# Optimization experiments

Measured on AMD Instinct MI355X. Metric: run time of the kernel, lower is better.

## Reference

```python
import jax, jax.numpy as jnp
import numpy as np

HID = 1024
HEADS = 16
HEAD_DIM = HID // HEADS
LN_EPS = 1e-5  # nn.LayerNorm default (module's self.eps is unused by its LayerNorms)


def layer_norm(x, w, b):
    m = jnp.mean(x, axis=-1, keepdims=True)
    v = jnp.mean(jnp.square(x - m), axis=-1, keepdims=True)
    return (x - m) * jax.lax.rsqrt(v + LN_EPS) * w + b


def setup_inputs() -> dict:
    key = jax.random.key(0)
    ks = jax.random.split(key, 12)
    B, Nq, Nk = 2, 1024, 4096
    s = 1.0 / np.sqrt(HID)
    inp = {
        "queries": jax.random.normal(ks[0], (B, Nq, HID), jnp.float32),
        "kv_tokens": jax.random.normal(ks[1], (B, Nk, HID), jnp.float32),
        "query_type_ids": jax.random.randint(ks[2], (Nq,), 0, 3),
        "kv_type_ids": jax.random.randint(ks[3], (Nk,), 0, 3),
        "kv_padding_mask": jax.random.randint(ks[4], (B, Nk), 0, 2).astype(bool).at[:, 0].set(True),
        "Wq": jax.random.normal(ks[5], (HID, HID), jnp.float32) * s,
        "Wk": jax.random.normal(ks[6], (HID, HID), jnp.float32) * s,
        "Wv": jax.random.normal(ks[7], (HID, HID), jnp.float32) * s,
        "Wo": jax.random.normal(ks[8], (HID, HID), jnp.float32) * s,
        "qn_w": jnp.ones((HID,), jnp.float32), "qn_b": jnp.zeros((HID,), jnp.float32),
        "kvn_w": jnp.ones((HID,), jnp.float32), "kvn_b": jnp.zeros((HID,), jnp.float32),
        "on_w": jnp.ones((HID,), jnp.float32), "on_b": jnp.zeros((HID,), jnp.float32),
        "typed_bias": jax.random.normal(ks[9], (3, 3), jnp.float32) * 0.1,
    }
    return inp


def reference(queries, kv_tokens, query_type_ids, kv_type_ids, kv_padding_mask,
              Wq, Wk, Wv, Wo, qn_w, qn_b, kvn_w, kvn_b, on_w, on_b, typed_bias):
    B, Nq, D = queries.shape
    Nk = kv_tokens.shape[1]
    qn = layer_norm(queries, qn_w, qn_b)
    kvn = layer_norm(kv_tokens, kvn_w, kvn_b)
    # projections (torch Linear: x @ W.T), split heads -> [B, N, H, hd]
    q = (qn @ Wq.T).reshape(B, Nq, HEADS, HEAD_DIM)
    k = (kvn @ Wk.T).reshape(B, Nk, HEADS, HEAD_DIM)
    v = (kvn @ Wv.T).reshape(B, Nk, HEADS, HEAD_DIM)
    scale = 1.0 / jnp.sqrt(jnp.asarray(HEAD_DIM, queries.dtype))
    scores = jnp.einsum("bqhd,bkhd->bhqk", q, k) * scale  # [B,H,Nq,Nk]
    # additive mask: typed bias gather [Nq,Nk] + padding neg-inf [B,Nk]
    tbias = typed_bias[query_type_ids][:, kv_type_ids]  # [Nq,Nk]
    neg_inf = jnp.finfo(queries.dtype).min
    pad = jnp.where(kv_padding_mask[:, None, None, :], jnp.asarray(0.0, queries.dtype), neg_inf)
    attn = jax.nn.softmax(scores + tbias[None, None] + pad, axis=-1)
    out = jnp.einsum("bhqk,bkhd->bqhd", attn, v).reshape(B, Nq, D)
    out = out @ Wo.T
    return layer_norm(queries + out, on_w, on_b)
```

## Files before the change

### kernel.cpp

```cpp
#include <hip/hip_runtime.h>
#include <hip/hip_bf16.h>

#define HID   1024
#define NQ    1024
#define NK    4096
#define BB    2
#define HEADS 16
#define HD    64
#define LN_EPS 1e-5f
#define NEG_BIG (-1e9f)
#define SOFT_C 16.0f
#define KSPLIT 4
#define NKS   (NK / KSPLIT)

typedef __bf16 bf16_t;
typedef bf16_t bf16x8 __attribute__((ext_vector_type(8)));
typedef bf16_t bf16x4 __attribute__((ext_vector_type(4)));
typedef float  f32x4  __attribute__((ext_vector_type(4)));

__device__ inline f32x4 mfma16(bf16x8 a, bf16x8 b, f32x4 c) {
    return __builtin_amdgcn_mfma_f32_16x16x32_bf16(a, b, c, 0, 0, 0);
}

__device__ inline void async_copy16(const bf16_t* g, bf16_t* l) {
    __builtin_amdgcn_global_load_lds(
        (const __attribute__((address_space(1))) void*)g,
        (__attribute__((address_space(3))) void*)l, 16, 0, 0);
}

__device__ inline void load8f(const void* p, int idx, int fl, float* o) {
    if (fl) {
        bf16x8 v = *(const bf16x8*)((const bf16_t*)p + idx);
#pragma unroll
        for (int i = 0; i < 8; i++) o[i] = (float)v[i];
    } else {
        float4 a = *(const float4*)((const float*)p + idx);
        float4 b = *(const float4*)((const float*)p + idx + 4);
        o[0] = a.x; o[1] = a.y; o[2] = a.z; o[3] = a.w;
        o[4] = b.x; o[5] = b.y; o[6] = b.z; o[7] = b.w;
    }
}
__device__ inline void load4f(const void* p, int idx, int fl, float* o) {
    if (fl) {
        bf16x4 v = *(const bf16x4*)((const bf16_t*)p + idx);
#pragma unroll
        for (int i = 0; i < 4; i++) o[i] = (float)v[i];
    } else {
        float4 a = *(const float4*)((const float*)p + idx);
        o[0] = a.x; o[1] = a.y; o[2] = a.z; o[3] = a.w;
    }
}

__global__ void detect_kernel(const void* __restrict__ qnw,
                              const void* __restrict__ pad,
                              int* __restrict__ flags) {
    __shared__ int bad;
    if (threadIdx.x == 0) bad = 0;
    __syncthreads();
    const unsigned int* pw = (const unsigned int*)pad;
    int any = 0;
    for (int i = threadIdx.x; i < 2048; i += 256)
        if (pw[i] > 1u) any = 1;
    if (any) atomicOr(&bad, 1);
    __syncthreads();
    if (threadIdx.x == 0) {
        flags[0] = (*(const unsigned int*)qnw == 0x3F803F80u) ? 1 : 0;
        flags[1] = bad;
    }
}

__device__ inline float2 block_sum2(float a, float b) {
#pragma unroll
    for (int off = 32; off > 0; off >>= 1) {
        a += __shfl_down(a, off, 64);
        b += __shfl_down(b, off, 64);
    }
    __shared__ float sm[8];
    int w = threadIdx.x >> 6;
    if ((threadIdx.x & 63) == 0) { sm[w] = a; sm[w + 4] = b; }
    __syncthreads();
    float sa = sm[0] + sm[1] + sm[2] + sm[3];
    float sb = sm[4] + sm[5] + sm[6] + sm[7];
    return make_float2(sa, sb);
}

__global__ __launch_bounds__(256) void norm_rows_kernel(const void* __restrict__ x,
                                                        const void* __restrict__ lnw,
                                                        const void* __restrict__ lnb,
                                                        bf16_t* __restrict__ out,
                                                        const int* __restrict__ flags) {
    int fl = flags[0];
    int row = blockIdx.x;
    int t = threadIdx.x;
    float xf[4];
    load4f(x, row * HID + t * 4, fl, xf);
    float s = 0.f, s2 = 0.f;
#pragma unroll
    for (int i = 0; i < 4; i++) { s += xf[i]; s2 += xf[i] * xf[i]; }
    float2 sums = block_sum2(s, s2);
    float mean = sums.x * (1.0f / HID);
    float var  = fmaxf(sums.y * (1.0f / HID) - mean * mean, 0.f);
    float inv  = rsqrtf(var + LN_EPS);
    float wv[4], bv[4];
    load4f(lnw, t * 4, fl, wv);
    load4f(lnb, t * 4, fl, bv);
    bf16x4 o;
#pragma unroll
    for (int i = 0; i < 4; i++)
        o[i] = (bf16_t)((xf[i] - mean) * inv * wv[i] + bv[i]);
    *(bf16x4*)(out + (size_t)row * HID + t * 4) = o;
}

__global__ __launch_bounds__(256) void wconv_kernel(const void* __restrict__ w0,
                                                    const void* __restrict__ w1,
                                                    const void* __restrict__ w2,
                                                    const void* __restrict__ w3,
                                                    bf16_t* __restrict__ out,
                                                    const int* __restrict__ flags) {
    int z = blockIdx.y;
    const void* in = (z == 0) ? w0 : (z == 1) ? w1 : (z == 2) ? w2 : w3;
    bf16_t* o = out + (size_t)z * HID * HID;
    int i = (blockIdx.x * 256 + threadIdx.x) * 8;
    if (flags[0]) {
        *(uint4*)(o + i) = *(const uint4*)((const bf16_t*)in + i);
    } else {
        float4 a = *(const float4*)((const float*)in + i);
        float4 b = *(const float4*)((const float*)in + i + 4);
        bf16x8 v;
        v[0] = (bf16_t)a.x; v[1] = (bf16_t)a.y; v[2] = (bf16_t)a.z; v[3] = (bf16_t)a.w;
        v[4] = (bf16_t)b.x; v[5] = (bf16_t)b.y; v[6] = (bf16_t)b.z; v[7] = (bf16_t)b.w;
        *(bf16x8*)(o + i) = v;
    }
}

__global__ __launch_bounds__(256) void final_ln_kernel(const void* __restrict__ q,
                                                       const float* __restrict__ o2a,
                                                       const float* __restrict__ o2b,
                                                       const void* __restrict__ w,
                                                       const void* __restrict__ bias,
                                                       void* __restrict__ y,
                                                       const int* __restrict__ flags) {
    int fl = flags[0];
    int row = blockIdx.x;
    int t = threadIdx.x;
    float qf[4];
    load4f(q, row * HID + t * 4, fl, qf);
    float4 oa = *(const float4*)(o2a + (size_t)row * HID + t * 4);
    float4 ob = *(const float4*)(o2b + (size_t)row * HID + t * 4);
    float xf[4] = { qf[0] + oa.x + ob.x, qf[1] + oa.y + ob.y,
                    qf[2] + oa.z + ob.z, qf[3] + oa.w + ob.w };
    float s = 0.f, s2 = 0.f;
#pragma unroll
    for (int i = 0; i < 4; i++) { s += xf[i]; s2 += xf[i] * xf[i]; }
    float2 sums = block_sum2(s, s2);
    float mean = sums.x * (1.0f / HID);
    float var  = fmaxf(sums.y * (1.0f / HID) - mean * mean, 0.f);
    float inv  = rsqrtf(var + LN_EPS);
    float wv[4], bv[4];
    load4f(w, t * 4, fl, wv);
    load4f(bias, t * 4, fl, bv);
    if (fl) {
        bf16x4 out;
#pragma unroll
        for (int i = 0; i < 4; i++)
            out[i] = (bf16_t)((xf[i] - mean) * inv * wv[i] + bv[i]);
        *(bf16x4*)((bf16_t*)y + (size_t)row * HID + t * 4) = out;
    } else {
        float4 out;
        out.x = (xf[0] - mean) * inv * wv[0] + bv[0];
        out.y = (xf[1] - mean) * inv * wv[1] + bv[1];
        out.z = (xf[2] - mean) * inv * wv[2] + bv[2];
        out.w = (xf[3] - mean) * inv * wv[3] + bv[3];
        *(float4*)((float*)y + (size_t)row * HID + t * 4) = out;
    }
}

__global__ __launch_bounds__(256) void maskc_kernel(const int* __restrict__ kt,
                                                    const void* __restrict__ pad,
                                                    const void* __restrict__ tb,
                                                    float* __restrict__ mc,
                                                    const int* __restrict__ flags) {
    int fl = flags[0], padbyte = flags[1];
    int i = blockIdx.x * 256 + threadIdx.x;
    int tq  = i / (BB * NK);
    int rem = i - tq * (BB * NK);
    int b   = rem >> 12;
    int key = rem & (NK - 1);
    int ti = tq * 3 + kt[key];
    float v = fl ? (float)((const bf16_t*)tb)[ti] : ((const float*)tb)[ti];
    v -= SOFT_C;
    bool ok = padbyte ? (((const unsigned char*)pad)[b * NK + key] != 0)
                      : (((const int*)pad)[b * NK + key] != 0);
    if (!ok) v = NEG_BIG;
    mc[i] = v;
}

__global__ __launch_bounds__(256) void gemm_qkv(const bf16_t* __restrict__ Aq,
                                                const bf16_t* __restrict__ Akv,
                                                const bf16_t* __restrict__ Wq,
                                                const bf16_t* __restrict__ Wkv,
                                                bf16_t* __restrict__ qp,
                                                bf16_t* __restrict__ kp,
                                                bf16_t* __restrict__ vT) {
    const int K = HID;
    __shared__ bf16_t As[128 * 32];
    __shared__ bf16_t Bs[128 * 32];
    int bid = blockIdx.x;
    bool isQ = bid < 128;
    const bf16_t* A; const bf16_t* W; int row0, col0;
    if (isQ) { A = Aq;  W = Wq;  row0 = (bid >> 3) * 128;  col0 = (bid & 7) * 128; }
    else     { int b2 = bid - 128;
               A = Akv; W = Wkv; row0 = (b2 >> 4) * 128;   col0 = (b2 & 15) * 128; }
    int t = threadIdx.x;
    int wave = t >> 6, lane = t & 63, quad = lane >> 4, l15 = lane & 15;
    int wr = wave >> 1, wc = wave & 1;

    int j0 = wave * 2;
    int srow = (lane >> 2);
    int skc  = (lane & 3) * 8;
    const bf16_t* Ag0 = A + (size_t)(row0 + 16 * j0 + srow) * K + skc;
    const bf16_t* Ag1 = Ag0 + (size_t)16 * K;
    const bf16_t* Bg0 = W + (size_t)(col0 + 16 * j0 + srow) * K + skc;
    const bf16_t* Bg1 = Bg0 + (size_t)16 * K;
    bf16_t* Asl0 = &As[j0 * 512];
    bf16_t* Asl1 = &As[j0 * 512 + 512];
    bf16_t* Bsl0 = &Bs[j0 * 512];
    bf16_t* Bsl1 = &Bs[j0 * 512 + 512];

    int aoff = (wr * 64 + l15) * 32 + quad * 8;
    int boff = (wc * 64 + l15) * 32 + quad * 8;

    f32x4 zero = {0.f, 0.f, 0.f, 0.f};
    f32x4 acc[4][4];
#pragma unroll
    for (int mt = 0; mt < 4; mt++)
#pragma unroll
        for (int nt = 0; nt < 4; nt++) acc[mt][nt] = zero;

    for (int k0 = 0; k0 < K; k0 += 32) {
        async_copy16(Ag0 + k0, Asl0);
        async_copy16(Ag1 + k0, Asl1);
        async_copy16(Bg0 + k0, Bsl0);
        async_copy16(Bg1 + k0, Bsl1);
        __syncthreads();
        bf16x8 a[4], b[4];
#pragma unroll
        for (int mt = 0; mt < 4; mt++) a[mt] = *(const bf16x8*)(&As[aoff + mt * 512]);
// ... 51 lines not shown
    int j0 = wave * 2;
    int srow = (lane >> 2);
    int skc  = (lane & 3) * 8;
    const bf16_t* Ag0 = A + (size_t)(row0 + 16 * j0 + srow) * K + skc;
    const bf16_t* Ag1 = Ag0 + (size_t)16 * K;
    const bf16_t* Bg0 = W + (size_t)(col0 + 16 * j0 + srow) * K + skc;
    const bf16_t* Bg1 = Bg0 + (size_t)16 * K;
    bf16_t* Asl0 = &As[j0 * 512];
    bf16_t* Asl1 = &As[j0 * 512 + 512];
    bf16_t* Bsl0 = &Bs[j0 * 512];
    bf16_t* Bsl1 = &Bs[j0 * 512 + 512];

    int aoff = (wr * 64 + l15) * 32 + quad * 8;
    int boff = (wc * 64 + l15) * 32 + quad * 8;

    f32x4 zero = {0.f, 0.f, 0.f, 0.f};
    f32x4 acc[4][4];
#pragma unroll
    for (int mt = 0; mt < 4; mt++)
#pragma unroll
        for (int nt = 0; nt < 4; nt++) acc[mt][nt] = zero;

    for (int k0 = kbeg; k0 < kend; k0 += 32) {
        async_copy16(Ag0 + k0, Asl0);
        async_copy16(Ag1 + k0, Asl1);
        async_copy16(Bg0 + k0, Bsl0);
        async_copy16(Bg1 + k0, Bsl1);
        __syncthreads();
        bf16x8 a[4], b[4];
#pragma unroll
        for (int mt = 0; mt < 4; mt++) a[mt] = *(const bf16x8*)(&As[aoff + mt * 512]);
#pragma unroll
        for (int nt = 0; nt < 4; nt++) b[nt] = *(const bf16x8*)(&Bs[boff + nt * 512]);
#pragma unroll
        for (int mt = 0; mt < 4; mt++)
#pragma unroll
            for (int nt = 0; nt < 4; nt++)
                acc[mt][nt] = mfma16(a[mt], b[nt], acc[mt][nt]);
        __syncthreads();
    }

#pragma unroll
    for (int mt = 0; mt < 4; mt++)
#pragma unroll
        for (int nt = 0; nt < 4; nt++) {
            int gr = row0 + wr * 64 + mt * 16 + quad * 4;
            int gc = col0 + wc * 64 + nt * 16 + l15;
#pragma unroll
            for (int r = 0; r < 4; r++)
                Co[(size_t)(gr + r) * HID + gc] = acc[mt][nt][r];
        }
}

__global__ __launch_bounds__(256) void attn_kernel(const bf16_t* __restrict__ q,
                                                   const bf16_t* __restrict__ kmat,
                                                   const bf16_t* __restrict__ vT,
                                                   const int* __restrict__ qt,
                                                   const float* __restrict__ mc,
                                                   bf16_t* __restrict__ Opart,
                                                   float* __restrict__ lpart) {
    int q0 = blockIdx.x * 64;
    int h  = blockIdx.y;
    int zz = blockIdx.z;
    int b  = zz >> 2;
    int split = zz & (KSPLIT - 1);
    int t = threadIdx.x, wave = t >> 6, lane = t & 63, quad = lane >> 4, l15 = lane & 15;

    __shared__ bf16_t Ks[2][64 * 64];
    __shared__ bf16_t Vs[2][64 * 64];

    const bf16_t* qbase = q + ((size_t)(b * NQ + q0 + wave * 16 + l15)) * HID + h * HD + quad * 8;
    bf16x8 aq0 = *(const bf16x8*)(qbase);
    bf16x8 aq1 = *(const bf16x8*)(qbase + 32);

    int qi = q0 + wave * 16 + l15;
    const float* mrow = mc + ((size_t)qt[qi] * BB + b) * NK;

    f32x4 zero = {0.f, 0.f, 0.f, 0.f};
    f32x4 O[4] = {zero, zero, zero, zero};
    float l_ = 0.f;

    int kt_beg = split * NKS;

    int srow = wave * 16 + (lane >> 2);
    int sc2  = (lane & 3) * 2;
    int vsw = srow & 7;
    int vl0 = srow * 64 + ((sc2)     ^ vsw) * 8;
    int vl1 = srow * 64 + ((sc2 + 1) ^ vsw) * 8;
    int prow = (srow & 0x23) | ((srow & 4) << 2) | ((srow >> 1) & 0x0C);
    int ksw = prow & 7;
    int kl0 = prow * 64 + ((sc2)     ^ ksw) * 8;
    int kl1 = prow * 64 + ((sc2 + 1) ^ ksw) * 8;

    const bf16_t* kgp = kmat + ((size_t)(b * NK + kt_beg + srow)) * HID + h * HD + sc2 * 8;
    const bf16_t* vgp = vT + ((size_t)(b * HID + h * HD + srow)) * NK + kt_beg + sc2 * 8;

    int fx = l15 & 7;
    int fA = l15 * 64 + ((quad) ^ fx) * 8;
    int fB = l15 * 64 + ((quad | 4) ^ fx) * 8;

    {
        uint4 ka = *(const uint4*)(kgp), kb = *(const uint4*)(kgp + 8);
        uint4 va = *(const uint4*)(vgp), vb = *(const uint4*)(vgp + 8);
        *(uint4*)&Ks[0][kl0] = ka; *(uint4*)&Ks[0][kl1] = kb;
        *(uint4*)&Vs[0][vl0] = va; *(uint4*)&Vs[0][vl1] = vb;
        kgp += 64 * HID; vgp += 64;
    }

    for (int it = 0; it < NKS / 64; ++it) {
        int cur = it & 1;
        __syncthreads();
        bool more = (it + 1 < NKS / 64);
        uint4 ka, kb, va, vb;
        if (more) {
            ka = *(const uint4*)(kgp); kb = *(const uint4*)(kgp + 8);
            va = *(const uint4*)(vgp); vb = *(const uint4*)(vgp + 8);
            kgp += 64 * HID; vgp += 64;
        }
        int kt0 = kt_beg + it * 64;
        float4 mk4[4];
#pragma unroll
        for (int nt = 0; nt < 4; nt++)
            mk4[nt] = *(const float4*)(mrow + kt0 + ((nt >> 1) << 5) + (quad << 3) + ((nt & 1) << 2));
        const bf16_t* Kc = Ks[cur];
        const bf16_t* Vc = Vs[cur];
        f32x4 s4[4] = {zero, zero, zero, zero};
#pragma unroll
        for (int nt = 0; nt < 4; nt++) {
            bf16x8 k0 = *(const bf16x8*)(Kc + nt * 1024 + fA);
            bf16x8 k1 = *(const bf16x8*)(Kc + nt * 1024 + fB);
            s4[nt] = mfma16(k0, aq0, s4[nt]);
            s4[nt] = mfma16(k1, aq1, s4[nt]);
        }
        bf16x8 pa0, pa1;
#pragma unroll
        for (int nt = 0; nt < 4; nt++) {
            const float* mkp = (const float*)&mk4[nt];
#pragma unroll
            for (int r = 0; r < 4; r++) {
                float p = __expf(fmaf(s4[nt][r], 0.125f, mkp[r]));
                l_ += p;
                bf16_t pb = (bf16_t)p;
                if (nt == 0)      pa0[r]     = pb;
                else if (nt == 1) pa0[r + 4] = pb;
                else if (nt == 2) pa1[r]     = pb;
                else              pa1[r + 4] = pb;
            }
        }
#pragma unroll
        for (int dt = 0; dt < 4; dt++) {
            bf16x8 v0 = *(const bf16x8*)(Vc + dt * 1024 + fA);
            bf16x8 v1 = *(const bf16x8*)(Vc + dt * 1024 + fB);
            O[dt] = mfma16(v0, pa0, O[dt]);
            O[dt] = mfma16(v1, pa1, O[dt]);
        }
        if (more) {
            int nxt = cur ^ 1;
            *(uint4*)&Ks[nxt][kl0] = ka; *(uint4*)&Ks[nxt][kl1] = kb;
            *(uint4*)&Vs[nxt][vl0] = va; *(uint4*)&Vs[nxt][vl1] = vb;
        }
    }

    size_t srow_base = (size_t)((split * BB + b) * HEADS + h) * NQ;
    float lf = l_;
    lf += __shfl_xor(lf, 16, 64);
    lf += __shfl_xor(lf, 32, 64);
    if (quad == 0) lpart[srow_base + qi] = lf;

    bf16_t* ob = &Ks[0][0] + wave * 1024;
#pragma unroll
    for (int dt = 0; dt < 4; dt++) {
        bf16x4 ov;
#pragma unroll
        for (int r = 0; r < 4; r++) ov[r] = (bf16_t)O[dt][r];
        *(bf16x4*)(ob + l15 * 64 + (((dt * 2 + (quad >> 1)) ^ fx) << 3) + ((quad & 1) << 2)) = ov;
    }
    int qq = lane >> 2, cc = lane & 3, sx = qq & 7;
    bf16x8 r0 = *(const bf16x8*)(ob + qq * 64 + (((cc * 2)     ^ sx) << 3));
    bf16x8 r1 = *(const bf16x8*)(ob + qq * 64 + (((cc * 2 + 1) ^ sx) << 3));
    size_t orow = (srow_base + (size_t)(q0 + wave * 16 + qq)) * HD + cc * 16;
    *(uint4*)(Opart + orow)     = *(uint4*)&r0;
    *(uint4*)(Opart + orow + 8) = *(uint4*)&r1;
}

__global__ __launch_bounds__(256) void combine_kernel(const bf16_t* __restrict__ Opart,
                                                      const float* __restrict__ lpart,
                                                      bf16_t* __restrict__ ctx) {
    int wave = threadIdx.x >> 6, lane = threadIdx.x & 63;
    int rid = blockIdx.x * 4 + wave;
    int b   = rid >> 14;
    int rem = rid & 16383;
    int h   = rem >> 10;
    int qi  = rem & 1023;
    float o = 0.f, l = 0.f;
#pragma unroll
    for (int s = 0; s < KSPLIT; s++) {
        size_t idx = (size_t)((s * BB + b) * HEADS + h) * NQ + qi;
        l += lpart[idx];
        o += (float)Opart[idx * HD + lane];
    }
    ctx[(size_t)(b * NQ + qi) * HID + h * HD + lane] = (bf16_t)(o / l);
}

extern "C" void kernel_launch(void* const* d_in, const int* in_sizes, int n_in,
                              void* d_out, int out_size, void* d_ws, size_t ws_size,
                              hipStream_t stream) {
    (void)in_sizes; (void)n_in; (void)out_size; (void)ws_size;
    const void* queries = d_in[0];
    const void* kv      = d_in[1];
    const int* qt       = (const int*)d_in[2];
    const int* kt       = (const int*)d_in[3];
    const void* pad     = d_in[4];
    const void* Wq   = d_in[5];
    const void* Wk   = d_in[6];
    const void* Wv   = d_in[7];
    const void* Wo   = d_in[8];
    const void* qn_w = d_in[9];
    const void* qn_b = d_in[10];
    const void* kvn_w = d_in[11];
    const void* kvn_b = d_in[12];
    const void* on_w = d_in[13];
    const void* on_b = d_in[14];
    const void* tb   = d_in[15];

    char* ws = (char*)d_ws;
    bf16_t* q_c  = (bf16_t*)(ws);
    bf16_t* kv_c = (bf16_t*)(ws + ((size_t)4  << 20));
    bf16_t* ctx  = (bf16_t*)(ws + ((size_t)4  << 20));
    bf16_t* Wq_c = (bf16_t*)(ws + ((size_t)20 << 20));
    bf16_t* Wk_c = (bf16_t*)(ws + ((size_t)22 << 20));
    bf16_t* Wv_c = (bf16_t*)(ws + ((size_t)24 << 20));
    bf16_t* Wo_c = (bf16_t*)(ws + ((size_t)26 << 20));
    bf16_t* qp   = (bf16_t*)(ws + ((size_t)28 << 20));
    bf16_t* kp   = (bf16_t*)(ws + ((size_t)32 << 20));
    float*  o2a  = (float*)(ws + ((size_t)32 << 20));
    float*  o2b  = (float*)(ws + ((size_t)40 << 20));
    bf16_t* vT   = (bf16_t*)(ws + ((size_t)48 << 20));
    float*  mc   = (float*)(ws + ((size_t)64 << 20));
    int*    flags = (int*)(ws + ((size_t)64 << 20) + (256 << 10));
    bf16_t* Opart = (bf16_t*)(ws + ((size_t)65 << 20));
    float*  lbuf  = (float*)(ws + ((size_t)82 << 20));

    detect_kernel<<<1, 256, 0, stream>>>(qn_w, pad, flags);
    norm_rows_kernel<<<BB * NQ, 256, 0, stream>>>(queries, qn_w, qn_b, q_c, flags);
    norm_rows_kernel<<<BB * NK, 256, 0, stream>>>(kv, kvn_w, kvn_b, kv_c, flags);
    wconv_kernel<<<dim3(512, 4), 256, 0, stream>>>(Wq, Wk, Wv, Wo, Wq_c, flags);
    maskc_kernel<<<(3 * BB * NK) / 256, 256, 0, stream>>>(kt, pad, tb, mc, flags);
    gemm_qkv<<<1152, 256, 0, stream>>>(q_c, kv_c, Wq_c, Wk_c, qp, kp, vT);
    attn_kernel<<<dim3(NQ / 64, HEADS, BB * KSPLIT), 256, 0, stream>>>(qp, kp, vT, qt, mc, Opart, lbuf);
    combine_kernel<<<(BB * HEADS * NQ) / 4, 256, 0, stream>>>(Opart, lbuf, ctx);
    gemm_o<<<dim3(16, 8, 2), 256, 0, stream>>>(ctx, Wo_c, o2a, o2b);
    final_ln_kernel<<<BB * NQ, 256, 0, stream>>>(queries, o2a, o2b, on_w, on_b, d_out, flags);
}
```

Baseline: 278.0 us.

## Deepen attention K/V prefetch pipeline, remap blocks for XCD locality, use exp2

The attention kernel's K/V tile loop now keeps two tiles of loads in flight in registers, unrolled by two with ping-pong LDS buffers. Mask loads are prefetched one tile ahead, and a lighter LDS-wait-plus-barrier replaces __syncthreads. The grid is flattened to 1D and remapped so consecutive blocks on the same XCD share a (head, batch, split) group for L2 reuse of K/V. The softmax switches to exp2 with log2e folded into the scale and the mask constants, which adds register pressure in exchange for hiding global-load latency.

```diff
diff --git a/kernel.cpp b/kernel.cpp
--- a/kernel.cpp
+++ b/kernel.cpp
@@ -12,6 +12,8 @@
 #define SOFT_C 16.0f
 #define KSPLIT 4
 #define NKS   (NK / KSPLIT)
+#define LOG2E 1.4426950408889634f
+#define QSCALE_L2E 0.18033688f
 
 typedef __bf16 bf16_t;
 typedef bf16_t bf16x8 __attribute__((ext_vector_type(8)));
@@ -28,18 +30,6 @@
         (__attribute__((address_space(3))) void*)l, 16, 0, 0);
 }
 
-__device__ inline void load8f(const void* p, int idx, int fl, float* o) {
-    if (fl) {
-        bf16x8 v = *(const bf16x8*)((const bf16_t*)p + idx);
-#pragma unroll
-        for (int i = 0; i < 8; i++) o[i] = (float)v[i];
-    } else {
-        float4 a = *(const float4*)((const float*)p + idx);
-        float4 b = *(const float4*)((const float*)p + idx + 4);
-        o[0] = a.x; o[1] = a.y; o[2] = a.z; o[3] = a.w;
-        o[4] = b.x; o[5] = b.y; o[6] = b.z; o[7] = b.w;
-    }
-}
 __device__ inline void load4f(const void* p, int idx, int fl, float* o) {
     if (fl) {
         bf16x4 v = *(const bf16x4*)((const bf16_t*)p + idx);
@@ -188,7 +178,7 @@
     int key = rem & (NK - 1);
     int ti = tq * 3 + kt[key];
     float v = fl ? (float)((const bf16_t*)tb)[ti] : ((const float*)tb)[ti];
-    v -= SOFT_C;
+    v = (v - SOFT_C) * LOG2E;
     bool ok = padbyte ? (((const unsigned char*)pad)[b * NK + key] != 0)
                       : (((const int*)pad)[b * NK + key] != 0);
     if (!ok) v = NEG_BIG;
@@ -357,10 +347,12 @@
                                                    const float* __restrict__ mc,
                                                    bf16_t* __restrict__ Opart,
                                                    float* __restrict__ lpart) {
-    int q0 = blockIdx.x * 64;
-    int h  = blockIdx.y;
-    int zz = blockIdx.z;
-    int b  = zz >> 2;
+    int d   = blockIdx.x;
+    int idx = ((d & 7) << 8) | (d >> 3);
+    int q0  = (idx & 15) * 64;
+    int h   = (idx >> 4) & 15;
+    int zz  = idx >> 8;
+    int b   = zz >> 2;
     int split = zz & (KSPLIT - 1);
     int t = threadIdx.x, wave = t >> 6, lane = t & 63, quad = lane >> 4, l15 = lane & 15;
 
@@ -379,6 +371,7 @@
     float l_ = 0.f;
 
     int kt_beg = split * NKS;
+    const int NT = NKS / 64;
 
     int srow = wave * 16 + (lane >> 2);
     int sc2  = (lane & 3) * 2;
@@ -390,73 +383,95 @@
     int kl0 = prow * 64 + ((sc2)     ^ ksw) * 8;
     int kl1 = prow * 64 + ((sc2 + 1) ^ ksw) * 8;
 
-    const bf16_t* kgp = kmat + ((size_t)(b * NK + kt_beg + srow)) * HID + h * HD + sc2 * 8;
-    const bf16_t* vgp = vT + ((size_t)(b * HID + h * HD + srow)) * NK + kt_beg + sc2 * 8;
+    const bf16_t* kbase = kmat + ((size_t)(b * NK + kt_beg + srow)) * HID + h * HD + sc2 * 8;
+    const bf16_t* vbase = vT + ((size_t)(b * HID + h * HD + srow)) * NK + kt_beg + sc2 * 8;
+    const float*  mbase = mrow + kt_beg + (quad << 3);
 
     int fx = l15 & 7;
     int fA = l15 * 64 + ((quad) ^ fx) * 8;
     int fB = l15 * 64 + ((quad | 4) ^ fx) * 8;
 
-    {
-        uint4 ka = *(const uint4*)(kgp), kb = *(const uint4*)(kgp + 8);
-        uint4 va = *(const uint4*)(vgp), vb = *(const uint4*)(vgp + 8);
-        *(uint4*)&Ks[0][kl0] = ka; *(uint4*)&Ks[0][kl1] = kb;
-        *(uint4*)&Vs[0][vl0] = va; *(uint4*)&Vs[0][vl1] = vb;
-        kgp += 64 * HID; vgp += 64;
-    }
-
-    for (int it = 0; it < NKS / 64; ++it) {
-        int cur = it & 1;
-        __syncthreads();
-        bool more = (it + 1 < NKS / 64);
-        uint4 ka, kb, va, vb;
-        if (more) {
-            ka = *(const uint4*)(kgp); kb = *(const uint4*)(kgp + 8);
-            va = *(const uint4*)(vgp); vb = *(const uint4*)(vgp + 8);
-            kgp += 64 * HID; vgp += 64;
-        }
-        int kt0 = kt_beg + it * 64;
-        float4 mk4[4];
-#pragma unroll
-        for (int nt = 0; nt < 4; nt++)
-            mk4[nt] = *(const float4*)(mrow + kt0 + ((nt >> 1) << 5) + (quad << 3) + ((nt & 1) << 2));
-        const bf16_t* Kc = Ks[cur];
-        const bf16_t* Vc = Vs[cur];
-        f32x4 s4[4] = {zero, zero, zero, zero};
-#pragma unroll
-        for (int nt = 0; nt < 4; nt++) {
-            bf16x8 k0 = *(const bf16x8*)(Kc + nt * 1024 + fA);
-            bf16x8 k1 = *(const bf16x8*)(Kc + nt * 1024 + fB);
-            s4[nt] = mfma16(k0, aq0, s4[nt]);
-            s4[nt] = mfma16(k1, aq1, s4[nt]);
-        }
-        bf16x8 pa0, pa1;
-#pragma unroll
-        for (int nt = 0; nt < 4; nt++) {
-            const float* mkp = (const float*)&mk4[nt];
-#pragma unroll
-            for (int r = 0; r < 4; r++) {
-                float p = __expf(fmaf(s4[nt][r], 0.125f, mkp[r]));
-                l_ += p;
-                bf16_t pb = (bf16_t)p;
-                if (nt == 0)      pa0[r]     = pb;
-                else if (nt == 1) pa0[r + 4] = pb;
-                else if (nt == 2) pa1[r]     = pb;
-                else              pa1[r + 4] = pb;
-            }
-        }
-#pragma unroll
-        for (int dt = 0; dt < 4; dt++) {
-            bf16x8 v0 = *(const bf16x8*)(Vc + dt * 1024 + fA);
-            bf16x8 v1 = *(const bf16x8*)(Vc + dt * 1024 + fB);
-            O[dt] = mfma16(v0, pa0, O[dt]);
-            O[dt] = mfma16(v1, pa1, O[dt]);
-        }
-        if (more) {
-            int nxt = cur ^ 1;
-            *(uint4*)&Ks[nxt][kl0] = ka; *(uint4*)&Ks[nxt][kl1] = kb;
-            *(uint4*)&Vs[nxt][vl0] = va; *(uint4*)&Vs[nxt][vl1] = vb;
-        }
+    uint4 kA0, kA1, vA0, vA1;
+    uint4 kB0, kB1, vB0, vB1;
+    float4 mA[4], mB[4];
+
+#define PKV(K0, K1, V0, V1, IT)                                              \
+    if ((IT) < NT) {                                                         \
+        const bf16_t* kp_ = kbase + (size_t)(IT) * 64 * HID;                 \
+        const bf16_t* vp_ = vbase + (size_t)(IT) * 64;                       \
+        K0 = *(const uint4*)(kp_); K1 = *(const uint4*)(kp_ + 8);            \
+        V0 = *(const uint4*)(vp_); V1 = *(const uint4*)(vp_ + 8);            \
+    }
+#define PM(M, IT)                                                            \
+    if ((IT) < NT) {                                                         \
+        const float* mp_ = mbase + (size_t)(IT) * 64;                        \
+        M[0] = *(const float4*)(mp_);                                        \
+        M[1] = *(const float4*)(mp_ + 4);                                    \
+        M[2] = *(const float4*)(mp_ + 32);                                   \
+        M[3] = *(const float4*)(mp_ + 36);                                   \
+    }
+#define WKV(BUF, K0, K1, V0, V1, IT)                                         \
+    if ((IT) < NT) {                                                         \
+        *(uint4*)&Ks[BUF][kl0] = K0; *(uint4*)&Ks[BUF][kl1] = K1;            \
+        *(uint4*)&Vs[BUF][vl0] = V0; *(uint4*)&Vs[BUF][vl1] = V1;            \
+    }
+#define BAR()                                                                \
+    {                                                                        \
+        asm volatile("s_waitcnt lgkmcnt(0)" ::: "memory");                   \
+        __builtin_amdgcn_s_barrier();                                        \
+    }
+#define COMPUTE(BUF, M)                                                      \
+    {                                                                        \
+        const bf16_t* Kc = Ks[BUF];                                          \
+        const bf16_t* Vc = Vs[BUF];                                          \
+        f32x4 s4[4] = {zero, zero, zero, zero};                              \
+        _Pragma("unroll")                                                    \
+        for (int nt = 0; nt < 4; nt++) {                                     \
+            bf16x8 k0 = *(const bf16x8*)(Kc + nt * 1024 + fA);               \
+            bf16x8 k1 = *(const bf16x8*)(Kc + nt * 1024 + fB);               \
+            s4[nt] = mfma16(k0, aq0, s4[nt]);                                \
+            s4[nt] = mfma16(k1, aq1, s4[nt]);                                \
+        }                                                                    \
+        bf16x8 pa0, pa1;                                                     \
+        _Pragma("unroll")                                                    \
+        for (int nt = 0; nt < 4; nt++) {                                     \
+            const float* mkp = (const float*)&M[nt];                         \
+            _Pragma("unroll")                                                \
+            for (int r = 0; r < 4; r++) {                                    \
+                float p = exp2f(fmaf(s4[nt][r], QSCALE_L2E, mkp[r]));        \
+                l_ += p;                                                     \
+                bf16_t pb = (bf16_t)p;                                       \
+                if (nt == 0)      pa0[r]     = pb;                           \
+                else if (nt == 1) pa0[r + 4] = pb;                           \
+                else if (nt == 2) pa1[r]     = pb;                           \
+                else              pa1[r + 4] = pb;                           \
+            }                                                                \
+        }                                                                    \
+        _Pragma("unroll")                                                    \
+        for (int dt = 0; dt < 4; dt++) {                                     \
+            bf16x8 v0 = *(const bf16x8*)(Vc + dt * 1024 + fA);               \
+            bf16x8 v1 = *(const bf16x8*)(Vc + dt * 1024 + fB);               \
+            O[dt] = mfma16(v0, pa0, O[dt]);                                  \
+            O[dt] = mfma16(v1, pa1, O[dt]);                                  \
+        }                                                                    \
+    }
+
+    PKV(kA0, kA1, vA0, vA1, 0);
+    WKV(0, kA0, kA1, vA0, vA1, 0);
+    PKV(kB0, kB1, vB0, vB1, 1);
+    PM(mA, 0);
+
+    for (int it = 0; it < NT; it += 2) {
+        PM(mB, it + 1);
+        PKV(kA0, kA1, vA0, vA1, it + 2);
+        BAR();
+        COMPUTE(0, mA);
+        WKV(1, kB0, kB1, vB0, vB1, it + 1);
+        PM(mA, it + 2);
+        PKV(kB0, kB1, vB0, vB1, it + 3);
+        BAR();
+        COMPUTE(1, mB);
+        WKV(0, kA0, kA1, vA0, vA1, it + 2);
     }
 
     size_t srow_base = (size_t)((split * BB + b) * HEADS + h) * NQ;
@@ -479,6 +494,11 @@
     size_t orow = (srow_base + (size_t)(q0 + wave * 16 + qq)) * HD + cc * 16;
     *(uint4*)(Opart + orow)     = *(uint4*)&r0;
     *(uint4*)(Opart + orow + 8) = *(uint4*)&r1;
+#undef PKV
+#undef PM
+#undef WKV
+#undef BAR
+#undef COMPUTE
 }
 
 __global__ __launch_bounds__(256) void combine_kernel(const bf16_t* __restrict__ Opart,
@@ -545,7 +565,7 @@
     wconv_kernel<<<dim3(512, 4), 256, 0, stream>>>(Wq, Wk, Wv, Wo, Wq_c, flags);
     maskc_kernel<<<(3 * BB * NK) / 256, 256, 0, stream>>>(kt, pad, tb, mc, flags);
     gemm_qkv<<<1152, 256, 0, stream>>>(q_c, kv_c, Wq_c, Wk_c, qp, kp, vT);
-    attn_kernel<<<dim3(NQ / 64, HEADS, BB * KSPLIT), 256, 0, stream>>>(qp, kp, vT, qt, mc, Opart, lbuf);
+    attn_kernel<<<dim3((NQ / 64) * HEADS * BB * KSPLIT), 256, 0, stream>>>(qp, kp, vT, qt, mc, Opart, lbuf);
     combine_kernel<<<(BB * HEADS * NQ) / 4, 256, 0, stream>>>(Opart, lbuf, ctx);
     gemm_o<<<dim3(16, 8, 2), 256, 0, stream>>>(ctx, Wo_c, o2a, o2b);
     final_ln_kernel<<<BB * NQ, 256, 0, stream>>>(queries, o2a, o2b, on_w, on_b, d_out, flags);
```

After: 292.7 us. +5.3%, slower.

## Single-buffer attention LDS, remap blocks across XCDs, use exp2 and wave priority

Applied to the files above, without the earlier changes.

Attention now keeps K/V in a single LDS buffer: register-prefetched tiles are written to LDS between two raw barriers, which halves LDS use so that 8 blocks per CU can be requested in launch bounds. The grid is flattened and remapped so that consecutive blocks sharing the same head and split land on the same XCD, aiming for better L2 reuse of K/V. Softmax switches to exp2, with log2(e) folded into the mask constants and the score scale, and s_setprio raises wave priority around the MFMA sections. The cost is an extra barrier per iteration and less overlap between LDS writes and compute. The unused load8f helper is removed.

```diff
diff --git a/kernel.cpp b/kernel.cpp
--- a/kernel.cpp
+++ b/kernel.cpp
@@ -12,6 +12,8 @@
 #define SOFT_C 16.0f
 #define KSPLIT 4
 #define NKS   (NK / KSPLIT)
+#define LOG2E 1.4426950408889634f
+#define QSCALE_L2E 0.18033688f
 
 typedef __bf16 bf16_t;
 typedef bf16_t bf16x8 __attribute__((ext_vector_type(8)));
@@ -28,18 +30,6 @@
         (__attribute__((address_space(3))) void*)l, 16, 0, 0);
 }
 
-__device__ inline void load8f(const void* p, int idx, int fl, float* o) {
-    if (fl) {
-        bf16x8 v = *(const bf16x8*)((const bf16_t*)p + idx);
-#pragma unroll
-        for (int i = 0; i < 8; i++) o[i] = (float)v[i];
-    } else {
-        float4 a = *(const float4*)((const float*)p + idx);
-        float4 b = *(const float4*)((const float*)p + idx + 4);
-        o[0] = a.x; o[1] = a.y; o[2] = a.z; o[3] = a.w;
-        o[4] = b.x; o[5] = b.y; o[6] = b.z; o[7] = b.w;
-    }
-}
 __device__ inline void load4f(const void* p, int idx, int fl, float* o) {
     if (fl) {
         bf16x4 v = *(const bf16x4*)((const bf16_t*)p + idx);
@@ -188,7 +178,7 @@
     int key = rem & (NK - 1);
     int ti = tq * 3 + kt[key];
     float v = fl ? (float)((const bf16_t*)tb)[ti] : ((const float*)tb)[ti];
-    v -= SOFT_C;
+    v = (v - SOFT_C) * LOG2E;
     bool ok = padbyte ? (((const unsigned char*)pad)[b * NK + key] != 0)
                       : (((const int*)pad)[b * NK + key] != 0);
     if (!ok) v = NEG_BIG;
@@ -350,22 +340,24 @@
         }
 }
 
-__global__ __launch_bounds__(256) void attn_kernel(const bf16_t* __restrict__ q,
-                                                   const bf16_t* __restrict__ kmat,
-                                                   const bf16_t* __restrict__ vT,
-                                                   const int* __restrict__ qt,
-                                                   const float* __restrict__ mc,
-                                                   bf16_t* __restrict__ Opart,
-                                                   float* __restrict__ lpart) {
-    int q0 = blockIdx.x * 64;
-    int h  = blockIdx.y;
-    int zz = blockIdx.z;
-    int b  = zz >> 2;
+__global__ __launch_bounds__(256, 8) void attn_kernel(const bf16_t* __restrict__ q,
+                                                      const bf16_t* __restrict__ kmat,
+                                                      const bf16_t* __restrict__ vT,
+                                                      const int* __restrict__ qt,
+                                                      const float* __restrict__ mc,
+                                                      bf16_t* __restrict__ Opart,
+                                                      float* __restrict__ lpart) {
+    int d   = blockIdx.x;
+    int idx = ((d & 7) << 8) | (d >> 3);
+    int q0  = (idx & 15) * 64;
+    int h   = (idx >> 4) & 15;
+    int zz  = idx >> 8;
+    int b   = zz >> 2;
     int split = zz & (KSPLIT - 1);
     int t = threadIdx.x, wave = t >> 6, lane = t & 63, quad = lane >> 4, l15 = lane & 15;
 
-    __shared__ bf16_t Ks[2][64 * 64];
-    __shared__ bf16_t Vs[2][64 * 64];
+    __shared__ bf16_t Ks[64 * 64];
+    __shared__ bf16_t Vs[64 * 64];
 
     const bf16_t* qbase = q + ((size_t)(b * NQ + q0 + wave * 16 + l15)) * HID + h * HD + quad * 8;
     bf16x8 aq0 = *(const bf16x8*)(qbase);
@@ -379,64 +371,64 @@
     float l_ = 0.f;
 
     int kt_beg = split * NKS;
+    const int NT = NKS / 64;
 
     int srow = wave * 16 + (lane >> 2);
     int sc2  = (lane & 3) * 2;
     int vsw = srow & 7;
-    int vl0 = srow * 64 + ((sc2)     ^ vsw) * 8;
-    int vl1 = srow * 64 + ((sc2 + 1) ^ vsw) * 8;
+    int vl0 = srow * 64 + ((sc2) ^ vsw) * 8;
+    int vl1 = vl0 ^ 8;
     int prow = (srow & 0x23) | ((srow & 4) << 2) | ((srow >> 1) & 0x0C);
     int ksw = prow & 7;
-    int kl0 = prow * 64 + ((sc2)     ^ ksw) * 8;
-    int kl1 = prow * 64 + ((sc2 + 1) ^ ksw) * 8;
+    int kl0 = prow * 64 + ((sc2) ^ ksw) * 8;
+    int kl1 = kl0 ^ 8;
 
     const bf16_t* kgp = kmat + ((size_t)(b * NK + kt_beg + srow)) * HID + h * HD + sc2 * 8;
     const bf16_t* vgp = vT + ((size_t)(b * HID + h * HD + srow)) * NK + kt_beg + sc2 * 8;
+    const float*  mbase = mrow + kt_beg + (quad << 3);
 
     int fx = l15 & 7;
     int fA = l15 * 64 + ((quad) ^ fx) * 8;
-    int fB = l15 * 64 + ((quad | 4) ^ fx) * 8;
-
-    {
-        uint4 ka = *(const uint4*)(kgp), kb = *(const uint4*)(kgp + 8);
-        uint4 va = *(const uint4*)(vgp), vb = *(const uint4*)(vgp + 8);
-        *(uint4*)&Ks[0][kl0] = ka; *(uint4*)&Ks[0][kl1] = kb;
-        *(uint4*)&Vs[0][vl0] = va; *(uint4*)&Vs[0][vl1] = vb;
-        kgp += 64 * HID; vgp += 64;
-    }
-
-    for (int it = 0; it < NKS / 64; ++it) {
-        int cur = it & 1;
-        __syncthreads();
-        bool more = (it + 1 < NKS / 64);
-        uint4 ka, kb, va, vb;
-        if (more) {
+    int fB = fA ^ 32;
+
+    uint4 ka = *(const uint4*)(kgp), kb = *(const uint4*)(kgp + 8);
+    uint4 va = *(const uint4*)(vgp), vb = *(const uint4*)(vgp + 8);
+    kgp += 64 * HID; vgp += 64;
+
+    for (int it = 0; it < NT; ++it) {
+        __builtin_amdgcn_s_barrier();
+        *(uint4*)&Ks[kl0] = ka; *(uint4*)&Ks[kl1] = kb;
+        *(uint4*)&Vs[vl0] = va; *(uint4*)&Vs[vl1] = vb;
+        asm volatile("s_waitcnt lgkmcnt(0)" ::: "memory");
+        __builtin_amdgcn_s_barrier();
+        if (it + 1 < NT) {
             ka = *(const uint4*)(kgp); kb = *(const uint4*)(kgp + 8);
             va = *(const uint4*)(vgp); vb = *(const uint4*)(vgp + 8);
             kgp += 64 * HID; vgp += 64;
         }
-        int kt0 = kt_beg + it * 64;
+        const float* mp = mbase + it * 64;
         float4 mk4[4];
-#pragma unroll
-        for (int nt = 0; nt < 4; nt++)
-            mk4[nt] = *(const float4*)(mrow + kt0 + ((nt >> 1) << 5) + (quad << 3) + ((nt & 1) << 2));
-        const bf16_t* Kc = Ks[cur];
-        const bf16_t* Vc = Vs[cur];
+        mk4[0] = *(const float4*)(mp);
+        mk4[1] = *(const float4*)(mp + 4);
+        mk4[2] = *(const float4*)(mp + 32);
+        mk4[3] = *(const float4*)(mp + 36);
         f32x4 s4[4] = {zero, zero, zero, zero};
+        __builtin_amdgcn_s_setprio(1);
 #pragma unroll
         for (int nt = 0; nt < 4; nt++) {
-            bf16x8 k0 = *(const bf16x8*)(Kc + nt * 1024 + fA);
-            bf16x8 k1 = *(const bf16x8*)(Kc + nt * 1024 + fB);
+            bf16x8 k0 = *(const bf16x8*)(Ks + nt * 1024 + fA);
+            bf16x8 k1 = *(const bf16x8*)(Ks + nt * 1024 + fB);
             s4[nt] = mfma16(k0, aq0, s4[nt]);
             s4[nt] = mfma16(k1, aq1, s4[nt]);
         }
+        __builtin_amdgcn_s_setprio(0);
         bf16x8 pa0, pa1;
 #pragma unroll
         for (int nt = 0; nt < 4; nt++) {
             const float* mkp = (const float*)&mk4[nt];
 #pragma unroll
             for (int r = 0; r < 4; r++) {
-                float p = __expf(fmaf(s4[nt][r], 0.125f, mkp[r]));
+                float p = exp2f(fmaf(s4[nt][r], QSCALE_L2E, mkp[r]));
                 l_ += p;
                 bf16_t pb = (bf16_t)p;
                 if (nt == 0)      pa0[r]     = pb;
@@ -445,18 +437,15 @@
                 else              pa1[r + 4] = pb;
             }
         }
+        __builtin_amdgcn_s_setprio(1);
 #pragma unroll
         for (int dt = 0; dt < 4; dt++) {
-            bf16x8 v0 = *(const bf16x8*)(Vc + dt * 1024 + fA);
-            bf16x8 v1 = *(const bf16x8*)(Vc + dt * 1024 + fB);
+            bf16x8 v0 = *(const bf16x8*)(Vs + dt * 1024 + fA);
+            bf16x8 v1 = *(const bf16x8*)(Vs + dt * 1024 + fB);
             O[dt] = mfma16(v0, pa0, O[dt]);
             O[dt] = mfma16(v1, pa1, O[dt]);
         }
-        if (more) {
-            int nxt = cur ^ 1;
-            *(uint4*)&Ks[nxt][kl0] = ka; *(uint4*)&Ks[nxt][kl1] = kb;
-            *(uint4*)&Vs[nxt][vl0] = va; *(uint4*)&Vs[nxt][vl1] = vb;
-        }
+        __builtin_amdgcn_s_setprio(0);
     }
 
     size_t srow_base = (size_t)((split * BB + b) * HEADS + h) * NQ;
@@ -465,7 +454,8 @@
     lf += __shfl_xor(lf, 32, 64);
     if (quad == 0) lpart[srow_base + qi] = lf;
 
-    bf16_t* ob = &Ks[0][0] + wave * 1024;
+    __syncthreads();
+    bf16_t* ob = &Ks[0] + wave * 1024;
 #pragma unroll
     for (int dt = 0; dt < 4; dt++) {
         bf16x4 ov;
@@ -545,7 +535,7 @@
     wconv_kernel<<<dim3(512, 4), 256, 0, stream>>>(Wq, Wk, Wv, Wo, Wq_c, flags);
     maskc_kernel<<<(3 * BB * NK) / 256, 256, 0, stream>>>(kt, pad, tb, mc, flags);
     gemm_qkv<<<1152, 256, 0, stream>>>(q_c, kv_c, Wq_c, Wk_c, qp, kp, vT);
-    attn_kernel<<<dim3(NQ / 64, HEADS, BB * KSPLIT), 256, 0, stream>>>(qp, kp, vT, qt, mc, Opart, lbuf);
+    attn_kernel<<<dim3((NQ / 64) * HEADS * BB * KSPLIT), 256, 0, stream>>>(qp, kp, vT, qt, mc, Opart, lbuf);
     combine_kernel<<<(BB * HEADS * NQ) / 4, 256, 0, stream>>>(Opart, lbuf, ctx);
     gemm_o<<<dim3(16, 8, 2), 256, 0, stream>>>(ctx, Wo_c, o2a, o2b);
     final_ln_kernel<<<BB * NQ, 256, 0, stream>>>(queries, o2a, o2b, on_w, on_b, d_out, flags);
```

New measurement: 537.1 us. 1.93x slower.

## Fuse prep kernels into one launch, use exp2 softmax, split attention by batch

Applied to the files above, without the earlier changes.

Merges the detect, both layernorm passes, the weight conversion and the mask-construction kernels into a single prep kernel. Dtype detection now happens inline in each kernel instead of through a flags buffer, which removes several launches and the serial dependency on the detect kernel. The mask is prescaled by log2(e) so the softmax can use exp2f with a folded scale constant. Attention is now launched as two half-size grids, one per batch, which adds a launch and may lower occupancy per grid.

```diff
diff --git a/kernel.cpp b/kernel.cpp
--- a/kernel.cpp
+++ b/kernel.cpp
@@ -12,6 +12,8 @@
 #define SOFT_C 16.0f
 #define KSPLIT 4
 #define NKS   (NK / KSPLIT)
+#define LOG2E 1.4426950408889634f
+#define QSCALE_L2E 0.18033688f
 
 typedef __bf16 bf16_t;
 typedef bf16_t bf16x8 __attribute__((ext_vector_type(8)));
@@ -28,18 +30,10 @@
         (__attribute__((address_space(3))) void*)l, 16, 0, 0);
 }
 
-__device__ inline void load8f(const void* p, int idx, int fl, float* o) {
-    if (fl) {
-        bf16x8 v = *(const bf16x8*)((const bf16_t*)p + idx);
-#pragma unroll
-        for (int i = 0; i < 8; i++) o[i] = (float)v[i];
-    } else {
-        float4 a = *(const float4*)((const float*)p + idx);
-        float4 b = *(const float4*)((const float*)p + idx + 4);
-        o[0] = a.x; o[1] = a.y; o[2] = a.z; o[3] = a.w;
-        o[4] = b.x; o[5] = b.y; o[6] = b.z; o[7] = b.w;
-    }
-}
+__device__ inline int probe_bf16(const void* qnw) {
+    return (*(const unsigned int*)qnw == 0x3F803F80u) ? 1 : 0;
+}
+
 __device__ inline void load4f(const void* p, int idx, int fl, float* o) {
     if (fl) {
         bf16x4 v = *(const bf16x4*)((const bf16_t*)p + idx);
@@ -48,24 +42,6 @@
     } else {
         float4 a = *(const float4*)((const float*)p + idx);
         o[0] = a.x; o[1] = a.y; o[2] = a.z; o[3] = a.w;
-    }
-}
-
-__global__ void detect_kernel(const void* __restrict__ qnw,
-                              const void* __restrict__ pad,
-                              int* __restrict__ flags) {
-    __shared__ int bad;
-    if (threadIdx.x == 0) bad = 0;
-    __syncthreads();
-    const unsigned int* pw = (const unsigned int*)pad;
-    int any = 0;
-    for (int i = threadIdx.x; i < 2048; i += 256)
-        if (pw[i] > 1u) any = 1;
-    if (any) atomicOr(&bad, 1);
-    __syncthreads();
-    if (threadIdx.x == 0) {
-        flags[0] = (*(const unsigned int*)qnw == 0x3F803F80u) ? 1 : 0;
-        flags[1] = bad;
     }
 }
 
@@ -84,115 +60,91 @@
     return make_float2(sa, sb);
 }
 
-__global__ __launch_bounds__(256) void norm_rows_kernel(const void* __restrict__ x,
-                                                        const void* __restrict__ lnw,
-                                                        const void* __restrict__ lnb,
-                                                        bf16_t* __restrict__ out,
-                                                        const int* __restrict__ flags) {
-    int fl = flags[0];
-    int row = blockIdx.x;
+__global__ __launch_bounds__(256) void prep_kernel(const void* __restrict__ queries,
+                                                   const void* __restrict__ kv,
+                                                   const void* __restrict__ qn_w,
+                                                   const void* __restrict__ qn_b,
+                                                   const void* __restrict__ kvn_w,
+                                                   const void* __restrict__ kvn_b,
+                                                   bf16_t* __restrict__ q_c,
+                                                   bf16_t* __restrict__ kv_c,
+                                                   const void* __restrict__ w0,
+                                                   const void* __restrict__ w1,
+                                                   const void* __restrict__ w2,
+                                                   const void* __restrict__ w3,
+                                                   bf16_t* __restrict__ wout,
+                                                   const int* __restrict__ kt,
+                                                   const void* __restrict__ pad,
+                                                   const void* __restrict__ tb,
+                                                   float* __restrict__ mc) {
+    int fl = probe_bf16(qn_w);
+    int blk = blockIdx.x;
     int t = threadIdx.x;
-    float xf[4];
-    load4f(x, row * HID + t * 4, fl, xf);
-    float s = 0.f, s2 = 0.f;
-#pragma unroll
-    for (int i = 0; i < 4; i++) { s += xf[i]; s2 += xf[i] * xf[i]; }
-    float2 sums = block_sum2(s, s2);
-    float mean = sums.x * (1.0f / HID);
-    float var  = fmaxf(sums.y * (1.0f / HID) - mean * mean, 0.f);
-    float inv  = rsqrtf(var + LN_EPS);
-    float wv[4], bv[4];
-    load4f(lnw, t * 4, fl, wv);
-    load4f(lnb, t * 4, fl, bv);
-    bf16x4 o;
-#pragma unroll
-    for (int i = 0; i < 4; i++)
-        o[i] = (bf16_t)((xf[i] - mean) * inv * wv[i] + bv[i]);
-    *(bf16x4*)(out + (size_t)row * HID + t * 4) = o;
-}
-
-__global__ __launch_bounds__(256) void wconv_kernel(const void* __restrict__ w0,
-                                                    const void* __restrict__ w1,
-                                                    const void* __restrict__ w2,
-                                                    const void* __restrict__ w3,
-                                                    bf16_t* __restrict__ out,
-                                                    const int* __restrict__ flags) {
-    int z = blockIdx.y;
-    const void* in = (z == 0) ? w0 : (z == 1) ? w1 : (z == 2) ? w2 : w3;
-    bf16_t* o = out + (size_t)z * HID * HID;
-    int i = (blockIdx.x * 256 + threadIdx.x) * 8;
-    if (flags[0]) {
-        *(uint4*)(o + i) = *(const uint4*)((const bf16_t*)in + i);
+    if (blk < BB * (NQ + NK)) {
+        bool isQ = blk < BB * NQ;
+        int row = isQ ? blk : blk - BB * NQ;
+        const void* x   = isQ ? queries : kv;
+        const void* lnw = isQ ? qn_w : kvn_w;
+        const void* lnb = isQ ? qn_b : kvn_b;
+        bf16_t* out = isQ ? q_c : kv_c;
+        float xf[4];
+        load4f(x, row * HID + t * 4, fl, xf);
+        float s = 0.f, s2 = 0.f;
+#pragma unroll
+        for (int i = 0; i < 4; i++) { s += xf[i]; s2 += xf[i] * xf[i]; }
+        float2 sums = block_sum2(s, s2);
+        float mean = sums.x * (1.0f / HID);
+        float var  = fmaxf(sums.y * (1.0f / HID) - mean * mean, 0.f);
+        float inv  = rsqrtf(var + LN_EPS);
+        float wv[4], bv[4];
+        load4f(lnw, t * 4, fl, wv);
+        load4f(lnb, t * 4, fl, bv);
+        bf16x4 o;
+#pragma unroll
+        for (int i = 0; i < 4; i++)
+            o[i] = (bf16_t)((xf[i] - mean) * inv * wv[i] + bv[i]);
+        *(bf16x4*)(out + (size_t)row * HID + t * 4) = o;
+    } else if (blk < BB * (NQ + NK) + 2048) {
+        int wb = blk - BB * (NQ + NK);
+        int z = wb >> 9;
+        const void* in = (z == 0) ? w0 : (z == 1) ? w1 : (z == 2) ? w2 : w3;
+        bf16_t* o = wout + (size_t)z * HID * HID;
+        int i = ((wb & 511) * 256 + t) * 8;
+        if (fl) {
+            *(uint4*)(o + i) = *(const uint4*)((const bf16_t*)in + i);
+        } else {
+            float4 a = *(const float4*)((const float*)in + i);
+            float4 b = *(const float4*)((const float*)in + i + 4);
+            bf16x8 v;
+            v[0] = (bf16_t)a.x; v[1] = (bf16_t)a.y; v[2] = (bf16_t)a.z; v[3] = (bf16_t)a.w;
+            v[4] = (bf16_t)b.x; v[5] = (bf16_t)b.y; v[6] = (bf16_t)b.z; v[7] = (bf16_t)b.w;
+            *(bf16x8*)(o + i) = v;
+        }
     } else {
-        float4 a = *(const float4*)((const float*)in + i);
-        float4 b = *(const float4*)((const float*)in + i + 4);
-        bf16x8 v;
-        v[0] = (bf16_t)a.x; v[1] = (bf16_t)a.y; v[2] = (bf16_t)a.z; v[3] = (bf16_t)a.w;
-        v[4] = (bf16_t)b.x; v[5] = (bf16_t)b.y; v[6] = (bf16_t)b.z; v[7] = (bf16_t)b.w;
-        *(bf16x8*)(o + i) = v;
-    }
-}
-
-__global__ __launch_bounds__(256) void final_ln_kernel(const void* __restrict__ q,
-                                                       const float* __restrict__ o2a,
-                                                       const float* __restrict__ o2b,
-                                                       const void* __restrict__ w,
-                                                       const void* __restrict__ bias,
-                                                       void* __restrict__ y,
-                                                       const int* __restrict__ flags) {
-    int fl = flags[0];
-    int row = blockIdx.x;
-    int t = threadIdx.x;
-    float qf[4];
-    load4f(q, row * HID + t * 4, fl, qf);
-    float4 oa = *(const float4*)(o2a + (size_t)row * HID + t * 4);
-    float4 ob = *(const float4*)(o2b + (size_t)row * HID + t * 4);
-    float xf[4] = { qf[0] + oa.x + ob.x, qf[1] + oa.y + ob.y,
-                    qf[2] + oa.z + ob.z, qf[3] + oa.w + ob.w };
-    float s = 0.f, s2 = 0.f;
-#pragma unroll
-    for (int i = 0; i < 4; i++) { s += xf[i]; s2 += xf[i] * xf[i]; }
-    float2 sums = block_sum2(s, s2);
-    float mean = sums.x * (1.0f / HID);
-    float var  = fmaxf(sums.y * (1.0f / HID) - mean * mean, 0.f);
-    float inv  = rsqrtf(var + LN_EPS);
-    float wv[4], bv[4];
-    load4f(w, t * 4, fl, wv);
-    load4f(bias, t * 4, fl, bv);
-    if (fl) {
-        bf16x4 out;
-#pragma unroll
-        for (int i = 0; i < 4; i++)
-            out[i] = (bf16_t)((xf[i] - mean) * inv * wv[i] + bv[i]);
-        *(bf16x4*)((bf16_t*)y + (size_t)row * HID + t * 4) = out;
-    } else {
-        float4 out;
-        out.x = (xf[0] - mean) * inv * wv[0] + bv[0];
-        out.y = (xf[1] - mean) * inv * wv[1] + bv[1];
-        out.z = (xf[2] - mean) * inv * wv[2] + bv[2];
-        out.w = (xf[3] - mean) * inv * wv[3] + bv[3];
-        *(float4*)((float*)y + (size_t)row * HID + t * 4) = out;
-    }
-}
-
-__global__ __launch_bounds__(256) void maskc_kernel(const int* __restrict__ kt,
-                                                    const void* __restrict__ pad,
-                                                    const void* __restrict__ tb,
-                                                    float* __restrict__ mc,
-                                                    const int* __restrict__ flags) {
-    int fl = flags[0], padbyte = flags[1];
-    int i = blockIdx.x * 256 + threadIdx.x;
-    int tq  = i / (BB * NK);
-    int rem = i - tq * (BB * NK);
-    int b   = rem >> 12;
-    int key = rem & (NK - 1);
-    int ti = tq * 3 + kt[key];
-    float v = fl ? (float)((const bf16_t*)tb)[ti] : ((const float*)tb)[ti];
-    v -= SOFT_C;
-    bool ok = padbyte ? (((const unsigned char*)pad)[b * NK + key] != 0)
-                      : (((const int*)pad)[b * NK + key] != 0);
-    if (!ok) v = NEG_BIG;
-    mc[i] = v;
+        __shared__ int bad;
+        if (t == 0) bad = 0;
+        __syncthreads();
+        const unsigned int* pw = (const unsigned int*)pad;
+        int any = 0;
+#pragma unroll
+        for (int j = 0; j < 8; j++)
+            if (pw[t * 8 + j] > 1u) any = 1;
+        if (any) atomicOr(&bad, 1);
+        __syncthreads();
+        int padbyte = bad;
+        int i = (blk - (BB * (NQ + NK) + 2048)) * 256 + t;
+        int tq  = i / (BB * NK);
+        int rem = i - tq * (BB * NK);
+        int b   = rem >> 12;
+        int key = rem & (NK - 1);
+        int ti = tq * 3 + kt[key];
+        float v = fl ? (float)((const bf16_t*)tb)[ti] : ((const float*)tb)[ti];
+        v = (v - SOFT_C) * LOG2E;
+        bool ok = padbyte ? (((const unsigned char*)pad)[b * NK + key] != 0)
+                          : (((const int*)pad)[b * NK + key] != 0);
+        if (!ok) v = NEG_BIG;
+        mc[i] = v;
+    }
 }
 
 __global__ __launch_bounds__(256) void gemm_qkv(const bf16_t* __restrict__ Aq,
@@ -356,10 +308,11 @@
                                                    const int* __restrict__ qt,
                                                    const float* __restrict__ mc,
                                                    bf16_t* __restrict__ Opart,
-                                                   float* __restrict__ lpart) {
+                                                   float* __restrict__ lpart,
+                                                   int zoff) {
     int q0 = blockIdx.x * 64;
     int h  = blockIdx.y;
-    int zz = blockIdx.z;
+    int zz = blockIdx.z + zoff;
     int b  = zz >> 2;
     int split = zz & (KSPLIT - 1);
     int t = threadIdx.x, wave = t >> 6, lane = t & 63, quad = lane >> 4, l15 = lane & 15;
@@ -436,7 +389,7 @@
             const float* mkp = (const float*)&mk4[nt];
 #pragma unroll
             for (int r = 0; r < 4; r++) {
-                float p = __expf(fmaf(s4[nt][r], 0.125f, mkp[r]));
+                float p = exp2f(fmaf(s4[nt][r], QSCALE_L2E, mkp[r]));
                 l_ += p;
                 bf16_t pb = (bf16_t)p;
                 if (nt == 0)      pa0[r]     = pb;
@@ -498,6 +451,47 @@
         o += (float)Opart[idx * HD + lane];
     }
     ctx[(size_t)(b * NQ + qi) * HID + h * HD + lane] = (bf16_t)(o / l);
+}
+
+__global__ __launch_bounds__(256) void final_ln_kernel(const void* __restrict__ q,
+                                                       const float* __restrict__ o2a,
+                                                       const float* __restrict__ o2b,
+                                                       const void* __restrict__ w,
+                                                       const void* __restrict__ bias,
+                                                       void* __restrict__ y) {
+    int fl = probe_bf16(w);
+    int row = blockIdx.x;
+    int t = threadIdx.x;
+    float qf[4];
+    load4f(q, row * HID + t * 4, fl, qf);
+    float4 oa = *(const float4*)(o2a + (size_t)row * HID + t * 4);
+    float4 ob = *(const float4*)(o2b + (size_t)row * HID + t * 4);
+    float xf[4] = { qf[0] + oa.x + ob.x, qf[1] + oa.y + ob.y,
+                    qf[2] + oa.z + ob.z, qf[3] + oa.w + ob.w };
+    float s = 0.f, s2 = 0.f;
+#pragma unroll
+    for (int i = 0; i < 4; i++) { s += xf[i]; s2 += xf[i] * xf[i]; }
+    float2 sums = block_sum2(s, s2);
+    float mean = sums.x * (1.0f / HID);
+    float var  = fmaxf(sums.y * (1.0f / HID) - mean * mean, 0.f);
+    float inv  = rsqrtf(var + LN_EPS);
+    float wv[4], bv[4];
+    load4f(w, t * 4, fl, wv);
+    load4f(bias, t * 4, fl, bv);
+    if (fl) {
+        bf16x4 out;
+#pragma unroll
+        for (int i = 0; i < 4; i++)
+            out[i] = (bf16_t)((xf[i] - mean) * inv * wv[i] + bv[i]);
+        *(bf16x4*)((bf16_t*)y + (size_t)row * HID + t * 4) = out;
+    } else {
+        float4 out;
+        out.x = (xf[0] - mean) * inv * wv[0] + bv[0];
+        out.y = (xf[1] - mean) * inv * wv[1] + bv[1];
+        out.z = (xf[2] - mean) * inv * wv[2] + bv[2];
+        out.w = (xf[3] - mean) * inv * wv[3] + bv[3];
+        *(float4*)((float*)y + (size_t)row * HID + t * 4) = out;
+    }
 }
 
 extern "C" void kernel_launch(void* const* d_in, const int* in_sizes, int n_in,
@@ -535,18 +529,16 @@
     float*  o2b  = (float*)(ws + ((size_t)40 << 20));
     bf16_t* vT   = (bf16_t*)(ws + ((size_t)48 << 20));
     float*  mc   = (float*)(ws + ((size_t)64 << 20));
-    int*    flags = (int*)(ws + ((size_t)64 << 20) + (256 << 10));
     bf16_t* Opart = (bf16_t*)(ws + ((size_t)65 << 20));
     float*  lbuf  = (float*)(ws + ((size_t)82 << 20));
 
-    detect_kernel<<<1, 256, 0, stream>>>(qn_w, pad, flags);
-    norm_rows_kernel<<<BB * NQ, 256, 0, stream>>>(queries, qn_w, qn_b, q_c, flags);
-    norm_rows_kernel<<<BB * NK, 256, 0, stream>>>(kv, kvn_w, kvn_b, kv_c, flags);
-    wconv_kernel<<<dim3(512, 4), 256, 0, stream>>>(Wq, Wk, Wv, Wo, Wq_c, flags);
-    maskc_kernel<<<(3 * BB * NK) / 256, 256, 0, stream>>>(kt, pad, tb, mc, flags);
+    prep_kernel<<<BB * (NQ + NK) + 2048 + 96, 256, 0, stream>>>(
+        queries, kv, qn_w, qn_b, kvn_w, kvn_b, q_c, kv_c,
+        Wq, Wk, Wv, Wo, Wq_c, kt, pad, tb, mc);
     gemm_qkv<<<1152, 256, 0, stream>>>(q_c, kv_c, Wq_c, Wk_c, qp, kp, vT);
-    attn_kernel<<<dim3(NQ / 64, HEADS, BB * KSPLIT), 256, 0, stream>>>(qp, kp, vT, qt, mc, Opart, lbuf);
+    attn_kernel<<<dim3(NQ / 64, HEADS, KSPLIT), 256, 0, stream>>>(qp, kp, vT, qt, mc, Opart, lbuf, 0);
+    attn_kernel<<<dim3(NQ / 64, HEADS, KSPLIT), 256, 0, stream>>>(qp, kp, vT, qt, mc, Opart, lbuf, KSPLIT);
     combine_kernel<<<(BB * HEADS * NQ) / 4, 256, 0, stream>>>(Opart, lbuf, ctx);
     gemm_o<<<dim3(16, 8, 2), 256, 0, stream>>>(ctx, Wo_c, o2a, o2b);
-    final_ln_kernel<<<BB * NQ, 256, 0, stream>>>(queries, o2a, o2b, on_w, on_b, d_out, flags);
-}
+    final_ln_kernel<<<BB * NQ, 256, 0, stream>>>(queries, o2a, o2b, on_w, on_b, d_out);
+}
```

New measurement: 273.4 us. Within noise of the previous version (-1.7%).
